# Kernel tuning notes

Measured on AMD Instinct MI355X. Metric: run time of the kernel, lower is better.

## Reference

```python
import jax, jax.numpy as jnp
import numpy as np
from jax import lax

NUM_CLASSES = 5
CONF_THRESH = 0.6
NMS_THRESH = 0.2
NUM_TOPK = 64          # min(topk=1000, 64) as in post_process
STRIDES = (8, 16, 32)
FMP = ((160, 160), (80, 80), (40, 40))  # 1280x1280 input
BATCH = 128


def setup_inputs() -> dict:
    key = jax.random.key(0)
    ks = jax.random.split(key, 9)
    d = {}
    i = 0
    for name, (h, w) in zip(("8", "16", "32"), FMP):
        hw = h * w
        d["obj" + name] = jax.random.normal(ks[i], (BATCH, hw, 1), jnp.float32); i += 1
        d["cls" + name] = jax.random.normal(ks[i], (BATCH, hw, NUM_CLASSES), jnp.float32); i += 1
        d["reg" + name] = jax.random.normal(ks[i], (BATCH, hw, 4), jnp.float32); i += 1
    return d


def make_anchors(h, w, stride):
    ay, ax = jnp.meshgrid(jnp.arange(h), jnp.arange(w), indexing="ij")
    xy = jnp.stack([ax, ay], axis=-1).astype(jnp.float32).reshape(-1, 2)
    return (xy + 0.5) * stride  # [HW, 2]


def decode_boxes(reg, anchors, stride):
    # ctr = reg[:, :2]*stride + anchor;  wh = exp(reg[:, 2:])*stride
    ctr = reg[:, :2] * stride + anchors
    wh = jnp.exp(reg[:, 2:]) * stride
    return jnp.concatenate([ctr - 0.5 * wh, ctr + 0.5 * wh], axis=-1)  # x1y1x2y2


def iou_matrix(b):
    # Faithful to YOLO.nms: areas un-clamped, intersection w/h clamped at 1e-10
    x1, y1, x2, y2 = b[:, 0], b[:, 1], b[:, 2], b[:, 3]
    areas = (x2 - x1) * (y2 - y1)
    xx1 = jnp.maximum(x1[:, None], x1[None, :])
    yy1 = jnp.maximum(y1[:, None], y1[None, :])
    xx2 = jnp.minimum(x2[:, None], x2[None, :])
    yy2 = jnp.minimum(y2[:, None], y2[None, :])
    w = jnp.maximum(1e-10, xx2 - xx1)
    h = jnp.maximum(1e-10, yy2 - yy1)
    inter = w * h
    return inter / (areas[:, None] + areas[None, :] - inter)


def nms_keep(iou, valid):
    # Greedy NMS on score-sorted candidates: fixed-length sequential suppression.
    n = iou.shape[0]
    idx = jnp.arange(n)
    def body(i, keep):
        sup = keep[i] & (iou[i] > NMS_THRESH) & (idx > i)
        return keep & jnp.logical_not(sup)
    return lax.fori_loop(0, n, body, valid)


def _single_image(obj8, cls8, reg8, obj16, cls16, reg16, obj32, cls32, reg32):
    levels = ((obj8, cls8, reg8), (obj16, cls16, reg16), (obj32, cls32, reg32))
    sc, lb, bx, vd = [], [], [], []
    for lvl, (obj, cls, reg) in enumerate(levels):
        h, w = FMP[lvl]
        s = STRIDES[lvl]
        anchors = make_anchors(h, w, s)
        boxes = decode_boxes(reg, anchors, s)                      # [HW, 4]
        scores = jnp.sqrt(jax.nn.sigmoid(obj) * jax.nn.sigmoid(cls)).reshape(-1)  # [HW*C]
        top_s, top_i = lax.top_k(scores, NUM_TOPK)
        a_idx = top_i // NUM_CLASSES
        labels = top_i % NUM_CLASSES
        sc.append(top_s)
        lb.append(labels)
        bx.append(boxes[a_idx])
        vd.append(top_s > CONF_THRESH)
    scores = jnp.concatenate(sc)          # [192]
    labels = jnp.concatenate(lb)
    boxes = jnp.concatenate(bx)           # [192, 4]
    valid = jnp.concatenate(vd)
    # Global score order (within each class this matches the per-class argsort)
    order = jnp.argsort(-scores)
    scores, labels, boxes, valid = scores[order], labels[order], boxes[order], valid[order]
    # Class-offset trick: boxes of different classes have IoU ~ 0 -> exactly per-class NMS
    off = labels.astype(jnp.float32) * (2.0 * jnp.max(jnp.abs(boxes)) + 1.0)
    keep = nms_keep(iou_matrix(boxes + off[:, None]), valid)
    scores = jnp.where(keep, scores, 0.0)
    boxes = jnp.where(keep[:, None], boxes, 0.0)
    labels = jnp.where(keep, labels, -1)
    return boxes, scores, labels


def reference(obj8, cls8, reg8, obj16, cls16, reg16, obj32, cls32, reg32):
    # Batched (vmapped) version of inference_single_image's decode+postprocess.
    # Returns fixed-size masked outputs: boxes [B,192,4], scores [B,192], labels [B,192].
    return jax.vmap(_single_image)(obj8, cls8, reg8, obj16, cls16, reg16, obj32, cls32, reg32)
```

## Files before the change

kernel.cpp:

```cpp
#include <hip/hip_runtime.h>


#define NUM_CLASSES 5
#define CONF_THRESH 0.6f
#define NMS_THRESH  0.2f
#define TOPK   64
#define BATCH  128
#define TOTK   192
#define NCH    21
#define CHUNK  1600
#define SCAP   2048
#define NTHR   320
#define WCAP   1600

typedef unsigned long long u64;
typedef unsigned int u32;

__device__ void bitonic_desc(u64* k, int m) {
  for (int kk = 2; kk <= m; kk <<= 1) {
    for (int j = kk >> 1; j > 0; j >>= 1) {
      __syncthreads();
      for (int i = threadIdx.x; i < m; i += blockDim.x) {
        int ixj = i ^ j;
        if (ixj > i) {
          u64 a = k[i], b = k[ixj];
          bool sw = ((i & kk) == 0) ? (a < b) : (a > b);
          if (sw) { k[i] = b; k[ixj] = a; }
        }
      }
    }
  }
  __syncthreads();
}

__device__ inline u32 wave_sort64_desc_u32(u32 v, int lane) {
  #pragma unroll
  for (int k = 2; k <= 64; k <<= 1) {
    #pragma unroll
    for (int j = k >> 1; j > 0; j >>= 1) {
      u32 o = __shfl_xor(v, j, 64);
      bool keepMax = (((lane & k) == 0) != ((lane & j) != 0));
      v = keepMax ? (v > o ? v : o) : (v < o ? v : o);
    }
  }
  return v;
}

__device__ inline u64 wave_sort64_desc(u64 v, int lane) {
  #pragma unroll
  for (int k = 2; k <= 64; k <<= 1) {
    #pragma unroll
    for (int j = k >> 1; j > 0; j >>= 1) {
      u64 o = __shfl_xor(v, j, 64);
      bool keepMax = (((lane & k) == 0) != ((lane & j) != 0));
      v = keepMax ? (v > o ? v : o) : (v < o ? v : o);
    }
  }
  return v;
}

__device__ __forceinline__ u64 u64max(u64 a, u64 b) { return a > b ? a : b; }
__device__ __forceinline__ u64 u64min(u64 a, u64 b) { return a < b ? a : b; }

__device__ __forceinline__ u64 bmerge64_desc(u64 v, int lane) {
  #pragma unroll
  for (int j = 32; j > 0; j >>= 1) {
    u64 o = __shfl_xor(v, j, 64);
    v = ((lane & j) == 0) ? u64max(v, o) : u64min(v, o);
  }
  return v;
}

__device__ __forceinline__ u64 merge_top64(u64 a, u64 brev, int lane) {
  return bmerge64_desc(u64max(a, brev), lane);
}

__device__ __forceinline__ u64 merge4_top64(u64 a, u64 brev, u64 c, u64 drev, int lane) {
  u64 ab = merge_top64(a, brev, lane);
  u64 cd = merge_top64(c, drev, lane);
  u64 cdr = __shfl(cd, 63 - lane, 64);
  return merge_top64(ab, cdr, lane);
}

__device__ inline u64 score_key(float so, float cv, int idx) {
  float sc = 1.0f / (1.0f + expf(-cv));
  float s  = sqrtf(__fmul_rn(so, sc));
  return ((u64)__float_as_uint(s) << 32) | (u32)(~(u32)idx);
}

__device__ inline float sigmoidf(float x) { return 1.0f / (1.0f + expf(-x)); }

__global__ __launch_bounds__(NTHR) void scan_kernel(
    const float* __restrict__ obj8,  const float* __restrict__ cls8,
    const float* __restrict__ obj16, const float* __restrict__ cls16,
    const float* __restrict__ obj32, const float* __restrict__ cls32,
    u64* __restrict__ ws_part) {
  __shared__ u64 keys[SCAP];
  __shared__ u32 wl[WCAP];
  __shared__ int cnt;
  __shared__ int wcnt;
  __shared__ u32 sthr[5];

  const int bx  = blockIdx.x;
  const int img = bx / NCH;
  const int c   = bx - img * NCH;
  const int t   = threadIdx.x;
  const int lane = t & 63, wv = t >> 6;

  const float *obj, *cls;
  int hw, off;
  if (c < 16)      { obj = obj8;  cls = cls8;  hw = 25600; off = c * CHUNK; }
  else if (c < 20) { obj = obj16; cls = cls16; hw = 6400;  off = (c - 16) * CHUNK; }
  else             { obj = obj32; cls = cls32; hw = 1600;  off = 0; }
  obj += (size_t)img * hw + off;
  cls += ((size_t)img * hw + off) * NUM_CLASSES;

  float ff[25];
  {
    const float4* c4 = (const float4*)cls + (size_t)t * 5;
    float4 q0 = c4[0], q1 = c4[1], q2 = c4[2], q3 = c4[3], q4 = c4[4];
    float4 ov = ((const float4*)obj)[t];
    float cv[20] = { q0.x,q0.y,q0.z,q0.w, q1.x,q1.y,q1.z,q1.w,
                     q2.x,q2.y,q2.z,q2.w, q3.x,q3.y,q3.z,q3.w,
                     q4.x,q4.y,q4.z,q4.w };
    float dob[4] = { 1.0f + __expf(-ov.x), 1.0f + __expf(-ov.y),
                     1.0f + __expf(-ov.z), 1.0f + __expf(-ov.w) };
    #pragma unroll
    for (int a = 0; a < 4; ++a)
      #pragma unroll
      for (int j = 0; j < 5; ++j)
        ff[a * 5 + j] = dob[a] * (1.0f + __expf(-cv[a * 5 + j]));
    float ot = obj[1280 + t];
    float dot_ = 1.0f + __expf(-ot);
    #pragma unroll
    for (int j = 0; j < 5; ++j) {
      float cvt = cls[(1280 + t) * 5 + j];
      ff[20 + j] = dot_ * (1.0f + __expf(-cvt));
    }
  }

  float pmin = ff[0];
  #pragma unroll
  for (int i = 1; i < 25; ++i) pmin = fminf(pmin, ff[i]);
  u32 srt = wave_sort64_desc_u32(__float_as_uint(pmin), lane);
  if (lane == 48) sthr[wv] = srt;
  if (t == 0) { cnt = 0; wcnt = 0; }
  __syncthreads();
  u64 thr; float thr_inv;
  {
    float pmax = __uint_as_float(sthr[0]);
    pmax = fmaxf(pmax, __uint_as_float(sthr[1]));
    pmax = fmaxf(pmax, __uint_as_float(sthr[2]));
    pmax = fmaxf(pmax, __uint_as_float(sthr[3]));
    pmax = fmaxf(pmax, __uint_as_float(sthr[4]));
    float ts = sqrtf(__fdiv_rn(1.0f, pmax)) * (1.0f - 1e-4f);
    thr = ((u64)__float_as_uint(ts) << 32) - 1ull;
    thr_inv = __fdiv_rn(1.0f, __fmul_rn(__fmul_rn(ts, ts), 1.0f - 2e-4f));
  }

  #pragma unroll
  for (int a = 0; a < 4; ++a)
    #pragma unroll
    for (int j = 0; j < 5; ++j)
      if (ff[a * 5 + j] <= thr_inv) {
        int p = atomicAdd(&wcnt, 1);
        if (p < WCAP) wl[p] = (u32)(((4 * t + a) << 3) | j);
      }
  #pragma unroll
  for (int j = 0; j < 5; ++j)
    if (ff[20 + j] <= thr_inv) {
      int p = atomicAdd(&wcnt, 1);
      if (p < WCAP) wl[p] = (u32)(((1280 + t) << 3) | j);
    }
  __syncthreads();
  const int wc = wcnt;

  if (wc <= WCAP) {
    for (int i = t; i < wc; i += NTHR) {
      u32 cd = wl[i];
      int al = (int)(cd >> 3);
      int jj = (int)(cd & 7u);
      float o   = obj[al];
      float cvv = cls[al * 5 + jj];
      u64 key = score_key(sigmoidf(o), cvv, (off + al) * NUM_CLASSES + jj);
      if (key > thr) { int p = atomicAdd(&cnt, 1); if (p < SCAP) keys[p] = key; }
    }
  } else {
    #pragma unroll
    for (int a = 0; a < 4; ++a)
      #pragma unroll
      for (int j = 0; j < 5; ++j)
        if (ff[a * 5 + j] <= thr_inv) {
          int al = 4 * t + a;
          u64 key = score_key(sigmoidf(obj[al]), cls[al * 5 + j],
                              (off + al) * NUM_CLASSES + j);
          if (key > thr) { int p = atomicAdd(&cnt, 1); if (p < SCAP) keys[p] = key; }
        }
    #pragma unroll
    for (int j = 0; j < 5; ++j)
      if (ff[20 + j] <= thr_inv) {
        int al = 1280 + t;
        u64 key = score_key(sigmoidf(obj[al]), cls[al * 5 + j],
                            (off + al) * NUM_CLASSES + j);
        if (key > thr) { int p = atomicAdd(&cnt, 1); if (p < SCAP) keys[p] = key; }
      }
  }
  __syncthreads();
  int cs = cnt; if (cs > SCAP) cs = SCAP;
  __syncthreads();

  if (cs > 512) {
    int m = 64; while (m < cs) m <<= 1;
    for (int i = cs + t; i < m; i += NTHR) keys[i] = 0ull;
    bitonic_desc(keys, m);
  } else {
    int npow = 1; while (npow * 64 < cs) npow <<= 1;
    for (int i = cs + t; i < npow * 64; i += NTHR) keys[i] = 0ull;
    __syncthreads();
    for (int r = wv; r < npow; r += 5) {
      u64 v = wave_sort64_desc(keys[r * 64 + lane], lane);
      keys[r * 64 + lane] = v;
    }
    __syncthreads();
    for (int half = npow >> 1; half >= 1; half >>= 1) {
      u64 res = 0ull;
      if (wv < half) {
        u64 a    = keys[(2 * wv) * 64 + lane];
        u64 brev = keys[(2 * wv + 1) * 64 + 63 - lane];
        res = merge_top64(a, brev, lane);
      }
      __syncthreads();
      if (wv < half) keys[wv * 64 + lane] = res;
      __syncthreads();
    }
  }
  if (t < TOPK) ws_part[(size_t)bx * TOPK + t] = keys[t];
}

__global__ __launch_bounds__(256) void merge_nms_kernel(
    const u64* __restrict__ ws_part,
    const float* __restrict__ reg8, const float* __restrict__ reg16, const float* __restrict__ reg32,
    float* __restrict__ out) {
  __shared__ u64   lds_runs[256];
  __shared__ u64   lvlkeys[TOTK];
  __shared__ u64   skeys[TOTK];
  __shared__ int   slb[TOTK];
  __shared__ float sbx[TOTK * 4];
  __shared__ float sX1[TOTK], sY1[TOTK], sX2[TOTK], sY2[TOTK], sA[TOTK];
  __shared__ u64   rows[TOTK * 3];
  __shared__ u64   svalid[3];
  __shared__ u64   skeep[3];
  __shared__ float lmarr[3];

  const int img  = blockIdx.x;
  const int t    = threadIdx.x;
  const int lane = t & 63, wv = t >> 6;

  const u64* pbase = ws_part + (size_t)img * NCH * TOPK;

  {
    const u64* q = pbase + (size_t)(4 * wv) * TOPK;
    u64 a    = q[lane];
    u64 brev = q[64 + 63 - lane];
    u64 c    = q[128 + lane];
    u64 drev = q[192 + 63 - lane];
    lds_runs[wv * 64 + lane] = merge4_top64(a, brev, c, drev, lane);
    if (wv == 3) lvlkeys[128 + lane] = pbase[20 * TOPK + lane];
  }
  __syncthreads();

  if (wv == 0) {
    u64 a    = lds_runs[lane];
    u64 brev = lds_runs[64 + 63 - lane];
    u64 c    = lds_runs[128 + lane];
    u64 drev = lds_runs[192 + 63 - lane];
    lvlkeys[lane] = merge4_top64(a, brev, c, drev, lane);
  } else if (wv == 1) {
    const u64* q = pbase + (size_t)16 * TOPK;
    u64 a    = q[lane];
    u64 brev = q[64 + 63 - lane];
    u64 c    = q[128 + lane];
    u64 drev = q[192 + 63 - lane];
    lvlkeys[64 + lane] = merge4_top64(a, brev, c, drev, lane);
  }
  __syncthreads();

  if (wv == 0) {
    const u64 HIMASK = 0xFFFFFFFF00000000ull;
    u64 s0 = (lvlkeys[lane] & HIMASK) | (u32)(~(u32)lane);
    int i1 = 64 + 63 - lane;
    u64 s1r = (lvlkeys[i1] & HIMASK) | (u32)(~(u32)i1);
    int i2 = 128 + 63 - lane;
    u64 s2r = (lvlkeys[i2] & HIMASK) | (u32)(~(u32)i2);
    u64 hi_ = bmerge64_desc(u64max(s0, s1r), lane);
    u64 lo_ = bmerge64_desc(u64min(s0, s1r), lane);
    u64 R1   = u64max(lo_, s2r);
    u64 out0 = bmerge64_desc(u64max(hi_, R1), lane);
    u64 out1 = bmerge64_desc(u64min(hi_, R1), lane);
    u64 out2 = bmerge64_desc(u64min(lo_, s2r), lane);
    skeys[lane]       = out0;
    skeys[64 + lane]  = out1;
    skeys[128 + lane] = out2;
  } else {
    int idx = t - 64;
    const float* reg; int w; int hw; float stride;
    if (wv == 1)      { reg = reg8;  w = 160; hw = 25600; stride = 8.0f;  }
    else if (wv == 2) { reg = reg16; w = 80;  hw = 6400;  stride = 16.0f; }
    else              { reg = reg32; w = 40;  hw = 1600;  stride = 32.0f; }
    reg += (size_t)img * hw * 4;
    u64 key = lvlkeys[idx];
    u32 raw = ~((u32)key);
    int a = (int)(raw / NUM_CLASSES);
    int c = (int)(raw - (u32)a * NUM_CLASSES);
    int ix = a % w, iy = a / w;
    float ax = __fmul_rn((float)ix + 0.5f, stride);
    float ay = __fmul_rn((float)iy + 0.5f, stride);
    float r0 = reg[a*4+0], r1 = reg[a*4+1], r2 = reg[a*4+2], r3 = reg[a*4+3];
    float cx = __fadd_rn(__fmul_rn(r0, stride), ax);
    float cy = __fadd_rn(__fmul_rn(r1, stride), ay);
    float wd = __fmul_rn(expf(r2), stride);
    float ht = __fmul_rn(expf(r3), stride);
    float x1 = __fsub_rn(cx, __fmul_rn(0.5f, wd));
    float y1 = __fsub_rn(cy, __fmul_rn(0.5f, ht));
    float x2 = __fadd_rn(cx, __fmul_rn(0.5f, wd));
    float y2 = __fadd_rn(cy, __fmul_rn(0.5f, ht));
    slb[idx] = c;
    sbx[idx*4+0] = x1; sbx[idx*4+1] = y1;
    sbx[idx*4+2] = x2; sbx[idx*4+3] = y2;
  }
  __syncthreads();

  float sc_r = 0.0f, b0 = 0.0f, b1 = 0.0f, b2 = 0.0f, b3 = 0.0f;
  int p = 0, lb_r = 0;
  if (t < TOTK) {
    u64 key = skeys[t];
    p = (int)(~((u32)key)) & 255;
    sc_r = __uint_as_float((u32)(key >> 32));
    lb_r = slb[p];
    b0 = sbx[p*4+0]; b1 = sbx[p*4+1]; b2 = sbx[p*4+2]; b3 = sbx[p*4+3];
    float lm = fmaxf(fmaxf(fabsf(b0), fabsf(b1)), fmaxf(fabsf(b2), fabsf(b3)));
    #pragma unroll
    for (int d = 32; d > 0; d >>= 1) lm = fmaxf(lm, __shfl_xor(lm, d, 64));
    if (lane == 0) lmarr[wv] = lm;
  }
  __syncthreads();

  const float lmAll = fmaxf(fmaxf(lmarr[0], lmarr[1]), lmarr[2]);
  const float offscale = __fadd_rn(__fmul_rn(2.0f, lmAll), 1.0f);

  float X1 = 0.0f, Y1 = 0.0f, X2 = 0.0f, Y2 = 0.0f, A = 0.0f;
  if (t < TOTK) {
    float off = __fmul_rn((float)lb_r, offscale);
    X1 = __fadd_rn(b0, off); Y1 = __fadd_rn(b1, off);
    X2 = __fadd_rn(b2, off); Y2 = __fadd_rn(b3, off);
    A  = __fmul_rn(__fsub_rn(X2, X1), __fsub_rn(Y2, Y1));
    sX1[t] = X1; sY1[t] = Y1; sX2[t] = X2; sY2[t] = Y2; sA[t] = A;
    u64 bal = __ballot(sc_r > CONF_THRESH);
    if (lane == 0) svalid[wv] = bal;
  }
  __syncthreads();

  if (t < TOTK) {
    u64 r0m = 0, r1m = 0, r2m = 0;
    for (int j = t + 1; j < TOTK; ++j) {
      float xx1 = fmaxf(X1, sX1[j]);
      float yy1 = fmaxf(Y1, sY1[j]);
      float xx2 = fminf(X2, sX2[j]);
      float yy2 = fminf(Y2, sY2[j]);
      float wv2 = fmaxf(1e-10f, __fsub_rn(xx2, xx1));
      float hv = fmaxf(1e-10f, __fsub_rn(yy2, yy1));
      float inter = __fmul_rn(wv2, hv);
      float den = __fsub_rn(__fadd_rn(A, sA[j]), inter);
      float iou = __fdiv_rn(inter, den);
      if (iou > NMS_THRESH) {
        u64 b = 1ull << (j & 63);
        int wd = j >> 6;
        r0m |= (wd == 0) ? b : 0ull;
        r1m |= (wd == 1) ? b : 0ull;
        r2m |= (wd == 2) ? b : 0ull;
      }
    }
    rows[t*3+0] = r0m; rows[t*3+1] = r1m; rows[t*3+2] = r2m;
  }
  __syncthreads();

  if (t < 64) {
    u64 k0 = svalid[0], k1 = svalid[1], k2 = svalid[2];
    #pragma unroll 4
    for (int i = 0; i < 64; ++i) {
      u64 m0 = rows[i*3+0], m1 = rows[i*3+1], m2 = rows[i*3+2];
      u64 sel = 0ull - ((k0 >> i) & 1ull);
      k0 &= ~(m0 & sel); k1 &= ~(m1 & sel); k2 &= ~(m2 & sel);
    }
    #pragma unroll 4
    for (int i = 0; i < 64; ++i) {
      int r = 64 + i;
      u64 m0 = rows[r*3+0], m1 = rows[r*3+1], m2 = rows[r*3+2];
      u64 sel = 0ull - ((k1 >> i) & 1ull);
      k0 &= ~(m0 & sel); k1 &= ~(m1 & sel); k2 &= ~(m2 & sel);
    }
    #pragma unroll 4
    for (int i = 0; i < 64; ++i) {
      int r = 128 + i;
      u64 m0 = rows[r*3+0], m1 = rows[r*3+1], m2 = rows[r*3+2];
      u64 sel = 0ull - ((k2 >> i) & 1ull);
      k0 &= ~(m0 & sel); k1 &= ~(m1 & sel); k2 &= ~(m2 & sel);
    }
    if (t == 0) { skeep[0] = k0; skeep[1] = k1; skeep[2] = k2; }
  }
  __syncthreads();

  if (t < TOTK) {
    float* out_boxes  = out;
    float* out_scores = out + (size_t)BATCH * TOTK * 4;
    float* out_labels = out + (size_t)BATCH * TOTK * 5;
    bool kp = (skeep[t >> 6] >> (t & 63)) & 1ull;
    int gi = img * TOTK + t;
    out_boxes[gi*4+0] = kp ? sbx[p*4+0] : 0.0f;
    out_boxes[gi*4+1] = kp ? sbx[p*4+1] : 0.0f;
    out_boxes[gi*4+2] = kp ? sbx[p*4+2] : 0.0f;
    out_boxes[gi*4+3] = kp ? sbx[p*4+3] : 0.0f;
    out_scores[gi] = kp ? sc_r : 0.0f;
    out_labels[gi] = kp ? (float)lb_r : -1.0f;
  }
}

extern "C" void kernel_launch(void* const* d_in, const int* in_sizes, int n_in,
                              void* d_out, int out_size, void* d_ws, size_t ws_size,
                              hipStream_t stream) {
  const float* obj8  = (const float*)d_in[0];
  const float* cls8  = (const float*)d_in[1];
  const float* reg8  = (const float*)d_in[2];
  const float* obj16 = (const float*)d_in[3];
  const float* cls16 = (const float*)d_in[4];
  const float* reg16 = (const float*)d_in[5];
  const float* obj32 = (const float*)d_in[6];
  const float* cls32 = (const float*)d_in[7];
  const float* reg32 = (const float*)d_in[8];

  u64* ws_part = (u64*)d_ws;

  scan_kernel<<<dim3(BATCH * NCH), dim3(NTHR), 0, stream>>>(
      obj8, cls8, obj16, cls16, obj32, cls32, ws_part);
  merge_nms_kernel<<<dim3(BATCH), dim3(256), 0, stream>>>(
      ws_part, reg8, reg16, reg32, (float*)d_out);
}
```

Baseline: 217.6 us.

## Fuse scan and merge-NMS kernels via last-block-per-image completion counter

Merges the per-chunk scan kernel and the per-image merge/NMS kernel into one launch. Each block writes its top-64 partial, bumps a per-image atomic counter, and the last block to finish for an image performs the merge, box decode and NMS. Shared memory for both phases is overlaid in a union. This removes the second kernel launch and the gap between kernels, at the cost of a memset launch, threadfence/atomic overhead, and a serialized tail block per image running at 320-thread occupancy.

Result: slower. 435.8 us (+100.3%).

```diff
diff --git a/kernel.cpp b/kernel.cpp
--- a/kernel.cpp
+++ b/kernel.cpp
@@ -16,22 +16,6 @@
 typedef unsigned long long u64;
 typedef unsigned int u32;
 
-__device__ void bitonic_desc(u64* k, int m) {
-  for (int kk = 2; kk <= m; kk <<= 1) {
-    for (int j = kk >> 1; j > 0; j >>= 1) {
-      __syncthreads();
-      for (int i = threadIdx.x; i < m; i += blockDim.x) {
-        int ixj = i ^ j;
-        if (ixj > i) {
-          u64 a = k[i], b = k[ixj];
-          bool sw = ((i & kk) == 0) ? (a < b) : (a > b);
-          if (sw) { k[i] = b; k[ixj] = a; }
-        }
-      }
-    }
-  }
-  __syncthreads();
-}
 
 __device__ inline u32 wave_sort64_desc_u32(u32 v, int lane) {
   #pragma unroll
@@ -90,16 +74,41 @@
 
 __device__ inline float sigmoidf(float x) { return 1.0f / (1.0f + expf(-x)); }
 
-__global__ __launch_bounds__(NTHR) void scan_kernel(
+
+struct MergeLds {
+  u64   lds_runs[256];
+  u64   lvlkeys[TOTK];
+  u64   skeys[TOTK];
+  int   slb[TOTK];
+  float sbx[TOTK * 4];
+  float sX1[TOTK], sY1[TOTK], sX2[TOTK], sY2[TOTK], sA[TOTK];
+  u64   rows[TOTK * 3];
+};
+struct ScanLds {
+  u64 keys[SCAP];
+  u32 wl[WCAP];
+};
+union SharedU {
+  ScanLds  s;
+  MergeLds m;
+};
+
+__global__ __launch_bounds__(NTHR) void yolo_fused(
     const float* __restrict__ obj8,  const float* __restrict__ cls8,
     const float* __restrict__ obj16, const float* __restrict__ cls16,
     const float* __restrict__ obj32, const float* __restrict__ cls32,
-    u64* __restrict__ ws_part) {
-  __shared__ u64 keys[SCAP];
-  __shared__ u32 wl[WCAP];
+    const float* __restrict__ reg8,  const float* __restrict__ reg16,
+    const float* __restrict__ reg32,
+    u64* __restrict__ ws_part, int* __restrict__ ready,
+    float* __restrict__ out) {
+  __shared__ SharedU u;
   __shared__ int cnt;
   __shared__ int wcnt;
   __shared__ u32 sthr[5];
+  __shared__ u64 svalid[3];
+  __shared__ u64 skeep[3];
+  __shared__ float lmarr[3];
+  __shared__ int tailflag;
 
   const int bx  = blockIdx.x;
   const int img = bx / NCH;
@@ -107,211 +116,218 @@
   const int t   = threadIdx.x;
   const int lane = t & 63, wv = t >> 6;
 
-  const float *obj, *cls;
-  int hw, off;
-  if (c < 16)      { obj = obj8;  cls = cls8;  hw = 25600; off = c * CHUNK; }
-  else if (c < 20) { obj = obj16; cls = cls16; hw = 6400;  off = (c - 16) * CHUNK; }
-  else             { obj = obj32; cls = cls32; hw = 1600;  off = 0; }
-  obj += (size_t)img * hw + off;
-  cls += ((size_t)img * hw + off) * NUM_CLASSES;
-
-  float ff[25];
   {
-    const float4* c4 = (const float4*)cls + (size_t)t * 5;
-    float4 q0 = c4[0], q1 = c4[1], q2 = c4[2], q3 = c4[3], q4 = c4[4];
-    float4 ov = ((const float4*)obj)[t];
-    float cv[20] = { q0.x,q0.y,q0.z,q0.w, q1.x,q1.y,q1.z,q1.w,
-                     q2.x,q2.y,q2.z,q2.w, q3.x,q3.y,q3.z,q3.w,
-                     q4.x,q4.y,q4.z,q4.w };
-    float dob[4] = { 1.0f + __expf(-ov.x), 1.0f + __expf(-ov.y),
-                     1.0f + __expf(-ov.z), 1.0f + __expf(-ov.w) };
-    #pragma unroll
-    for (int a = 0; a < 4; ++a)
+    const float *obj, *cls;
+    int hw, off;
+    if (c < 16)      { obj = obj8;  cls = cls8;  hw = 25600; off = c * CHUNK; }
+    else if (c < 20) { obj = obj16; cls = cls16; hw = 6400;  off = (c - 16) * CHUNK; }
+    else             { obj = obj32; cls = cls32; hw = 1600;  off = 0; }
+    obj += (size_t)img * hw + off;
+    cls += ((size_t)img * hw + off) * NUM_CLASSES;
+
+    float ff[25];
+    {
+      const float4* c4 = (const float4*)cls + (size_t)t * 5;
+      float4 q0 = c4[0], q1 = c4[1], q2 = c4[2], q3 = c4[3], q4 = c4[4];
+      float4 ov = ((const float4*)obj)[t];
+      float cv[20] = { q0.x,q0.y,q0.z,q0.w, q1.x,q1.y,q1.z,q1.w,
+                       q2.x,q2.y,q2.z,q2.w, q3.x,q3.y,q3.z,q3.w,
+                       q4.x,q4.y,q4.z,q4.w };
+      float dob[4] = { 1.0f + __expf(-ov.x), 1.0f + __expf(-ov.y),
+                       1.0f + __expf(-ov.z), 1.0f + __expf(-ov.w) };
       #pragma unroll
-      for (int j = 0; j < 5; ++j)
-        ff[a * 5 + j] = dob[a] * (1.0f + __expf(-cv[a * 5 + j]));
-    float ot = obj[1280 + t];
-    float dot_ = 1.0f + __expf(-ot);
-    #pragma unroll
-    for (int j = 0; j < 5; ++j) {
-      float cvt = cls[(1280 + t) * 5 + j];
-      ff[20 + j] = dot_ * (1.0f + __expf(-cvt));
-    }
-  }
-
-  float pmin = ff[0];
-  #pragma unroll
-  for (int i = 1; i < 25; ++i) pmin = fminf(pmin, ff[i]);
-  u32 srt = wave_sort64_desc_u32(__float_as_uint(pmin), lane);
-  if (lane == 48) sthr[wv] = srt;
-  if (t == 0) { cnt = 0; wcnt = 0; }
-  __syncthreads();
-  u64 thr; float thr_inv;
-  {
-    float pmax = __uint_as_float(sthr[0]);
-    pmax = fmaxf(pmax, __uint_as_float(sthr[1]));
-    pmax = fmaxf(pmax, __uint_as_float(sthr[2]));
-    pmax = fmaxf(pmax, __uint_as_float(sthr[3]));
-    pmax = fmaxf(pmax, __uint_as_float(sthr[4]));
-    float ts = sqrtf(__fdiv_rn(1.0f, pmax)) * (1.0f - 1e-4f);
-    thr = ((u64)__float_as_uint(ts) << 32) - 1ull;
-    thr_inv = __fdiv_rn(1.0f, __fmul_rn(__fmul_rn(ts, ts), 1.0f - 2e-4f));
-  }
-
-  #pragma unroll
-  for (int a = 0; a < 4; ++a)
-    #pragma unroll
-    for (int j = 0; j < 5; ++j)
-      if (ff[a * 5 + j] <= thr_inv) {
-        int p = atomicAdd(&wcnt, 1);
-        if (p < WCAP) wl[p] = (u32)(((4 * t + a) << 3) | j);
-      }
-  #pragma unroll
-  for (int j = 0; j < 5; ++j)
-    if (ff[20 + j] <= thr_inv) {
-      int p = atomicAdd(&wcnt, 1);
-      if (p < WCAP) wl[p] = (u32)(((1280 + t) << 3) | j);
-    }
-  __syncthreads();
-  const int wc = wcnt;
-
-  if (wc <= WCAP) {
-    for (int i = t; i < wc; i += NTHR) {
-      u32 cd = wl[i];
-      int al = (int)(cd >> 3);
-      int jj = (int)(cd & 7u);
-      float o   = obj[al];
-      float cvv = cls[al * 5 + jj];
-      u64 key = score_key(sigmoidf(o), cvv, (off + al) * NUM_CLASSES + jj);
-      if (key > thr) { int p = atomicAdd(&cnt, 1); if (p < SCAP) keys[p] = key; }
-    }
-  } else {
+      for (int a = 0; a < 4; ++a)
+        #pragma unroll
+        for (int j = 0; j < 5; ++j)
+          ff[a * 5 + j] = dob[a] * (1.0f + __expf(-cv[a * 5 + j]));
+      float ot = obj[1280 + t];
+      float dot_ = 1.0f + __expf(-ot);
+      #pragma unroll
+      for (int j = 0; j < 5; ++j) {
+        float cvt = cls[(1280 + t) * 5 + j];
+        ff[20 + j] = dot_ * (1.0f + __expf(-cvt));
+      }
+    }
+
+    float pmin = ff[0];
+    #pragma unroll
+    for (int i = 1; i < 25; ++i) pmin = fminf(pmin, ff[i]);
+    u32 srt = wave_sort64_desc_u32(__float_as_uint(pmin), lane);
+    if (lane == 48) sthr[wv] = srt;
+    if (t == 0) { cnt = 0; wcnt = 0; }
+    __syncthreads();
+    u64 thr; float thr_inv;
+    {
+      float pmax = __uint_as_float(sthr[0]);
+      pmax = fmaxf(pmax, __uint_as_float(sthr[1]));
+      pmax = fmaxf(pmax, __uint_as_float(sthr[2]));
+      pmax = fmaxf(pmax, __uint_as_float(sthr[3]));
+      pmax = fmaxf(pmax, __uint_as_float(sthr[4]));
+      float ts = sqrtf(__fdiv_rn(1.0f, pmax)) * (1.0f - 1e-4f);
+      thr = ((u64)__float_as_uint(ts) << 32) - 1ull;
+      thr_inv = __fdiv_rn(1.0f, __fmul_rn(__fmul_rn(ts, ts), 1.0f - 2e-4f));
+    }
+
     #pragma unroll
     for (int a = 0; a < 4; ++a)
       #pragma unroll
       for (int j = 0; j < 5; ++j)
         if (ff[a * 5 + j] <= thr_inv) {
-          int al = 4 * t + a;
+          int p = atomicAdd(&wcnt, 1);
+          if (p < WCAP) u.s.wl[p] = (u32)(((4 * t + a) << 3) | j);
+        }
+    #pragma unroll
+    for (int j = 0; j < 5; ++j)
+      if (ff[20 + j] <= thr_inv) {
+        int p = atomicAdd(&wcnt, 1);
+        if (p < WCAP) u.s.wl[p] = (u32)(((1280 + t) << 3) | j);
+      }
+    __syncthreads();
+    const int wc = wcnt;
+
+    if (wc <= WCAP) {
+      for (int i = t; i < wc; i += NTHR) {
+        u32 cd = u.s.wl[i];
+        int al = (int)(cd >> 3);
+        int jj = (int)(cd & 7u);
+        float o   = obj[al];
+        float cvv = cls[al * 5 + jj];
+        u64 key = score_key(sigmoidf(o), cvv, (off + al) * NUM_CLASSES + jj);
+        if (key > thr) { int p = atomicAdd(&cnt, 1); if (p < SCAP) u.s.keys[p] = key; }
+      }
+    } else {
+      #pragma unroll
+      for (int a = 0; a < 4; ++a)
+        #pragma unroll
+        for (int j = 0; j < 5; ++j)
+          if (ff[a * 5 + j] <= thr_inv) {
+            int al = 4 * t + a;
+            u64 key = score_key(sigmoidf(obj[al]), cls[al * 5 + j],
+                                (off + al) * NUM_CLASSES + j);
+            if (key > thr) { int p = atomicAdd(&cnt, 1); if (p < SCAP) u.s.keys[p] = key; }
+          }
+      #pragma unroll
+      for (int j = 0; j < 5; ++j)
+        if (ff[20 + j] <= thr_inv) {
+          int al = 1280 + t;
           u64 key = score_key(sigmoidf(obj[al]), cls[al * 5 + j],
                               (off + al) * NUM_CLASSES + j);
-          if (key > thr) { int p = atomicAdd(&cnt, 1); if (p < SCAP) keys[p] = key; }
+          if (key > thr) { int p = atomicAdd(&cnt, 1); if (p < SCAP) u.s.keys[p] = key; }
         }
-    #pragma unroll
-    for (int j = 0; j < 5; ++j)
-      if (ff[20 + j] <= thr_inv) {
-        int al = 1280 + t;
-        u64 key = score_key(sigmoidf(obj[al]), cls[al * 5 + j],
-                            (off + al) * NUM_CLASSES + j);
-        if (key > thr) { int p = atomicAdd(&cnt, 1); if (p < SCAP) keys[p] = key; }
-      }
-  }
-  __syncthreads();
-  int cs = cnt; if (cs > SCAP) cs = SCAP;
-  __syncthreads();
-
-  if (cs > 512) {
-    int m = 64; while (m < cs) m <<= 1;
-    for (int i = cs + t; i < m; i += NTHR) keys[i] = 0ull;
-    bitonic_desc(keys, m);
-  } else {
-    int npow = 1; while (npow * 64 < cs) npow <<= 1;
-    for (int i = cs + t; i < npow * 64; i += NTHR) keys[i] = 0ull;
+    }
     __syncthreads();
-    for (int r = wv; r < npow; r += 5) {
-      u64 v = wave_sort64_desc(keys[r * 64 + lane], lane);
-      keys[r * 64 + lane] = v;
-    }
+    int cs = cnt; if (cs > SCAP) cs = SCAP;
     __syncthreads();
-    for (int half = npow >> 1; half >= 1; half >>= 1) {
-      u64 res = 0ull;
-      if (wv < half) {
-        u64 a    = keys[(2 * wv) * 64 + lane];
-        u64 brev = keys[(2 * wv + 1) * 64 + 63 - lane];
-        res = merge_top64(a, brev, lane);
+
+    if (cs > 512) {
+      int m = 64; while (m < cs) m <<= 1;
+      for (int i = cs + t; i < m; i += NTHR) u.s.keys[i] = 0ull;
+      for (int kk = 2; kk <= m; kk <<= 1) {
+        for (int j = kk >> 1; j > 0; j >>= 1) {
+          __syncthreads();
+          for (int i = t; i < m; i += NTHR) {
+            int ixj = i ^ j;
+            if (ixj > i) {
+              u64 a = u.s.keys[i], b = u.s.keys[ixj];
+              bool sw = ((i & kk) == 0) ? (a < b) : (a > b);
+              if (sw) { u.s.keys[i] = b; u.s.keys[ixj] = a; }
+            }
+          }
+        }
       }
       __syncthreads();
-      if (wv < half) keys[wv * 64 + lane] = res;
+    } else {
+      int npow = 1; while (npow * 64 < cs) npow <<= 1;
+      for (int i = cs + t; i < npow * 64; i += NTHR) u.s.keys[i] = 0ull;
       __syncthreads();
-    }
-  }
-  if (t < TOPK) ws_part[(size_t)bx * TOPK + t] = keys[t];
-}
-
-__global__ __launch_bounds__(256) void merge_nms_kernel(
-    const u64* __restrict__ ws_part,
-    const float* __restrict__ reg8, const float* __restrict__ reg16, const float* __restrict__ reg32,
-    float* __restrict__ out) {
-  __shared__ u64   lds_runs[256];
-  __shared__ u64   lvlkeys[TOTK];
-  __shared__ u64   skeys[TOTK];
-  __shared__ int   slb[TOTK];
-  __shared__ float sbx[TOTK * 4];
-  __shared__ float sX1[TOTK], sY1[TOTK], sX2[TOTK], sY2[TOTK], sA[TOTK];
-  __shared__ u64   rows[TOTK * 3];
-  __shared__ u64   svalid[3];
-  __shared__ u64   skeep[3];
-  __shared__ float lmarr[3];
-
-  const int img  = blockIdx.x;
-  const int t    = threadIdx.x;
-  const int lane = t & 63, wv = t >> 6;
+      for (int r = wv; r < npow; r += 5) {
+        u64 v = wave_sort64_desc(u.s.keys[r * 64 + lane], lane);
+        u.s.keys[r * 64 + lane] = v;
+      }
+      __syncthreads();
+      for (int half = npow >> 1; half >= 1; half >>= 1) {
+        u64 res = 0ull;
+        if (wv < half) {
+          u64 a    = u.s.keys[(2 * wv) * 64 + lane];
+          u64 brev = u.s.keys[(2 * wv + 1) * 64 + 63 - lane];
+          res = merge_top64(a, brev, lane);
+        }
+        __syncthreads();
+        if (wv < half) u.s.keys[wv * 64 + lane] = res;
+        __syncthreads();
+      }
+    }
+    if (t < TOPK) ws_part[(size_t)bx * TOPK + t] = u.s.keys[t];
+  }
+
+  __syncthreads();
+  if (t == 0) {
+    __threadfence();
+    int old = atomicAdd(&ready[img], 1);
+    tailflag = (old == NCH - 1);
+  }
+  __syncthreads();
+  if (!tailflag) return;
+  __threadfence();
 
   const u64* pbase = ws_part + (size_t)img * NCH * TOPK;
 
-  {
+  __syncthreads();
+  if (wv < 4) {
     const u64* q = pbase + (size_t)(4 * wv) * TOPK;
     u64 a    = q[lane];
     u64 brev = q[64 + 63 - lane];
-    u64 c    = q[128 + lane];
+    u64 c2   = q[128 + lane];
     u64 drev = q[192 + 63 - lane];
-    lds_runs[wv * 64 + lane] = merge4_top64(a, brev, c, drev, lane);
-    if (wv == 3) lvlkeys[128 + lane] = pbase[20 * TOPK + lane];
+    u.m.lds_runs[wv * 64 + lane] = merge4_top64(a, brev, c2, drev, lane);
+  } else {
+    u.m.lvlkeys[128 + lane] = pbase[20 * TOPK + lane];
   }
   __syncthreads();
 
   if (wv == 0) {
-    u64 a    = lds_runs[lane];
-    u64 brev = lds_runs[64 + 63 - lane];
-    u64 c    = lds_runs[128 + lane];
-    u64 drev = lds_runs[192 + 63 - lane];
-    lvlkeys[lane] = merge4_top64(a, brev, c, drev, lane);
+    u64 a    = u.m.lds_runs[lane];
+    u64 brev = u.m.lds_runs[64 + 63 - lane];
+    u64 c2   = u.m.lds_runs[128 + lane];
+    u64 drev = u.m.lds_runs[192 + 63 - lane];
+    u.m.lvlkeys[lane] = merge4_top64(a, brev, c2, drev, lane);
   } else if (wv == 1) {
     const u64* q = pbase + (size_t)16 * TOPK;
     u64 a    = q[lane];
     u64 brev = q[64 + 63 - lane];
-    u64 c    = q[128 + lane];
+    u64 c2   = q[128 + lane];
     u64 drev = q[192 + 63 - lane];
-    lvlkeys[64 + lane] = merge4_top64(a, brev, c, drev, lane);
+    u.m.lvlkeys[64 + lane] = merge4_top64(a, brev, c2, drev, lane);
   }
   __syncthreads();
 
   if (wv == 0) {
     const u64 HIMASK = 0xFFFFFFFF00000000ull;
-    u64 s0 = (lvlkeys[lane] & HIMASK) | (u32)(~(u32)lane);
+    u64 s0 = (u.m.lvlkeys[lane] & HIMASK) | (u32)(~(u32)lane);
     int i1 = 64 + 63 - lane;
-    u64 s1r = (lvlkeys[i1] & HIMASK) | (u32)(~(u32)i1);
+    u64 s1r = (u.m.lvlkeys[i1] & HIMASK) | (u32)(~(u32)i1);
     int i2 = 128 + 63 - lane;
-    u64 s2r = (lvlkeys[i2] & HIMASK) | (u32)(~(u32)i2);
+    u64 s2r = (u.m.lvlkeys[i2] & HIMASK) | (u32)(~(u32)i2);
     u64 hi_ = bmerge64_desc(u64max(s0, s1r), lane);
     u64 lo_ = bmerge64_desc(u64min(s0, s1r), lane);
     u64 R1   = u64max(lo_, s2r);
     u64 out0 = bmerge64_desc(u64max(hi_, R1), lane);
     u64 out1 = bmerge64_desc(u64min(hi_, R1), lane);
     u64 out2 = bmerge64_desc(u64min(lo_, s2r), lane);
-    skeys[lane]       = out0;
-    skeys[64 + lane]  = out1;
-    skeys[128 + lane] = out2;
-  } else {
+    u.m.skeys[lane]       = out0;
+    u.m.skeys[64 + lane]  = out1;
+    u.m.skeys[128 + lane] = out2;
+  } else if (t >= 64 && t < 64 + TOTK) {
     int idx = t - 64;
     const float* reg; int w; int hw; float stride;
     if (wv == 1)      { reg = reg8;  w = 160; hw = 25600; stride = 8.0f;  }
     else if (wv == 2) { reg = reg16; w = 80;  hw = 6400;  stride = 16.0f; }
     else              { reg = reg32; w = 40;  hw = 1600;  stride = 32.0f; }
     reg += (size_t)img * hw * 4;
-    u64 key = lvlkeys[idx];
+    u64 key = u.m.lvlkeys[idx];
     u32 raw = ~((u32)key);
     int a = (int)(raw / NUM_CLASSES);
-    int c = (int)(raw - (u32)a * NUM_CLASSES);
+    int c2 = (int)(raw - (u32)a * NUM_CLASSES);
     int ix = a % w, iy = a / w;
     float ax = __fmul_rn((float)ix + 0.5f, stride);
     float ay = __fmul_rn((float)iy + 0.5f, stride);
@@ -324,20 +340,21 @@
     float y1 = __fsub_rn(cy, __fmul_rn(0.5f, ht));
     float x2 = __fadd_rn(cx, __fmul_rn(0.5f, wd));
     float y2 = __fadd_rn(cy, __fmul_rn(0.5f, ht));
-    slb[idx] = c;
-    sbx[idx*4+0] = x1; sbx[idx*4+1] = y1;
-    sbx[idx*4+2] = x2; sbx[idx*4+3] = y2;
+    u.m.slb[idx] = c2;
+    u.m.sbx[idx*4+0] = x1; u.m.sbx[idx*4+1] = y1;
+    u.m.sbx[idx*4+2] = x2; u.m.sbx[idx*4+3] = y2;
   }
   __syncthreads();
 
   float sc_r = 0.0f, b0 = 0.0f, b1 = 0.0f, b2 = 0.0f, b3 = 0.0f;
   int p = 0, lb_r = 0;
   if (t < TOTK) {
-    u64 key = skeys[t];
+    u64 key = u.m.skeys[t];
     p = (int)(~((u32)key)) & 255;
     sc_r = __uint_as_float((u32)(key >> 32));
-    lb_r = slb[p];
-    b0 = sbx[p*4+0]; b1 = sbx[p*4+1]; b2 = sbx[p*4+2]; b3 = sbx[p*4+3];
+    lb_r = u.m.slb[p];
+    b0 = u.m.sbx[p*4+0]; b1 = u.m.sbx[p*4+1];
+    b2 = u.m.sbx[p*4+2]; b3 = u.m.sbx[p*4+3];
     float lm = fmaxf(fmaxf(fabsf(b0), fabsf(b1)), fmaxf(fabsf(b2), fabsf(b3)));
     #pragma unroll
     for (int d = 32; d > 0; d >>= 1) lm = fmaxf(lm, __shfl_xor(lm, d, 64));
@@ -354,7 +371,8 @@
     X1 = __fadd_rn(b0, off); Y1 = __fadd_rn(b1, off);
     X2 = __fadd_rn(b2, off); Y2 = __fadd_rn(b3, off);
     A  = __fmul_rn(__fsub_rn(X2, X1), __fsub_rn(Y2, Y1));
-    sX1[t] = X1; sY1[t] = Y1; sX2[t] = X2; sY2[t] = Y2; sA[t] = A;
+    u.m.sX1[t] = X1; u.m.sY1[t] = Y1; u.m.sX2[t] = X2; u.m.sY2[t] = Y2;
+    u.m.sA[t] = A;
     u64 bal = __ballot(sc_r > CONF_THRESH);
     if (lane == 0) svalid[wv] = bal;
   }
@@ -363,14 +381,14 @@
   if (t < TOTK) {
     u64 r0m = 0, r1m = 0, r2m = 0;
     for (int j = t + 1; j < TOTK; ++j) {
-      float xx1 = fmaxf(X1, sX1[j]);
-      float yy1 = fmaxf(Y1, sY1[j]);
-      float xx2 = fminf(X2, sX2[j]);
-      float yy2 = fminf(Y2, sY2[j]);
+      float xx1 = fmaxf(X1, u.m.sX1[j]);
+      float yy1 = fmaxf(Y1, u.m.sY1[j]);
+      float xx2 = fminf(X2, u.m.sX2[j]);
+      float yy2 = fminf(Y2, u.m.sY2[j]);
       float wv2 = fmaxf(1e-10f, __fsub_rn(xx2, xx1));
       float hv = fmaxf(1e-10f, __fsub_rn(yy2, yy1));
       float inter = __fmul_rn(wv2, hv);
-      float den = __fsub_rn(__fadd_rn(A, sA[j]), inter);
+      float den = __fsub_rn(__fadd_rn(A, u.m.sA[j]), inter);
       float iou = __fdiv_rn(inter, den);
       if (iou > NMS_THRESH) {
         u64 b = 1ull << (j & 63);
@@ -380,7 +398,7 @@
         r2m |= (wd == 2) ? b : 0ull;
       }
     }
-    rows[t*3+0] = r0m; rows[t*3+1] = r1m; rows[t*3+2] = r2m;
+    u.m.rows[t*3+0] = r0m; u.m.rows[t*3+1] = r1m; u.m.rows[t*3+2] = r2m;
   }
   __syncthreads();
 
@@ -388,21 +406,21 @@
     u64 k0 = svalid[0], k1 = svalid[1], k2 = svalid[2];
     #pragma unroll 4
     for (int i = 0; i < 64; ++i) {
-      u64 m0 = rows[i*3+0], m1 = rows[i*3+1], m2 = rows[i*3+2];
+      u64 m0 = u.m.rows[i*3+0], m1 = u.m.rows[i*3+1], m2 = u.m.rows[i*3+2];
       u64 sel = 0ull - ((k0 >> i) & 1ull);
       k0 &= ~(m0 & sel); k1 &= ~(m1 & sel); k2 &= ~(m2 & sel);
     }
     #pragma unroll 4
     for (int i = 0; i < 64; ++i) {
       int r = 64 + i;
-      u64 m0 = rows[r*3+0], m1 = rows[r*3+1], m2 = rows[r*3+2];
+      u64 m0 = u.m.rows[r*3+0], m1 = u.m.rows[r*3+1], m2 = u.m.rows[r*3+2];
       u64 sel = 0ull - ((k1 >> i) & 1ull);
       k0 &= ~(m0 & sel); k1 &= ~(m1 & sel); k2 &= ~(m2 & sel);
     }
     #pragma unroll 4
     for (int i = 0; i < 64; ++i) {
       int r = 128 + i;
-      u64 m0 = rows[r*3+0], m1 = rows[r*3+1], m2 = rows[r*3+2];
+      u64 m0 = u.m.rows[r*3+0], m1 = u.m.rows[r*3+1], m2 = u.m.rows[r*3+2];
       u64 sel = 0ull - ((k2 >> i) & 1ull);
       k0 &= ~(m0 & sel); k1 &= ~(m1 & sel); k2 &= ~(m2 & sel);
     }
@@ -416,10 +434,10 @@
     float* out_labels = out + (size_t)BATCH * TOTK * 5;
     bool kp = (skeep[t >> 6] >> (t & 63)) & 1ull;
     int gi = img * TOTK + t;
-    out_boxes[gi*4+0] = kp ? sbx[p*4+0] : 0.0f;
-    out_boxes[gi*4+1] = kp ? sbx[p*4+1] : 0.0f;
-    out_boxes[gi*4+2] = kp ? sbx[p*4+2] : 0.0f;
-    out_boxes[gi*4+3] = kp ? sbx[p*4+3] : 0.0f;
+    out_boxes[gi*4+0] = kp ? u.m.sbx[p*4+0] : 0.0f;
+    out_boxes[gi*4+1] = kp ? u.m.sbx[p*4+1] : 0.0f;
+    out_boxes[gi*4+2] = kp ? u.m.sbx[p*4+2] : 0.0f;
+    out_boxes[gi*4+3] = kp ? u.m.sbx[p*4+3] : 0.0f;
     out_scores[gi] = kp ? sc_r : 0.0f;
     out_labels[gi] = kp ? (float)lb_r : -1.0f;
   }
@@ -439,9 +457,10 @@
   const float* reg32 = (const float*)d_in[8];
 
   u64* ws_part = (u64*)d_ws;
-
-  scan_kernel<<<dim3(BATCH * NCH), dim3(NTHR), 0, stream>>>(
-      obj8, cls8, obj16, cls16, obj32, cls32, ws_part);
-  merge_nms_kernel<<<dim3(BATCH), dim3(256), 0, stream>>>(
-      ws_part, reg8, reg16, reg32, (float*)d_out);
-}
+  int* ready   = (int*)((char*)d_ws + (size_t)BATCH * NCH * TOPK * sizeof(u64));
+
+  hipMemsetAsync(ready, 0, BATCH * sizeof(int), stream);
+  yolo_fused<<<dim3(BATCH * NCH), dim3(NTHR), 0, stream>>>(
+      obj8, cls8, obj16, cls16, obj32, cls32, reg8, reg16, reg32,
+      ws_part, ready, (float*)d_out);
+}
```
